# Performance work log

Hardware: AMD Instinct MI355X
Metric: run time of the kernel (lower is better)

Reference implementation:

```python
import jax, jax.numpy as jnp
import numpy as np

B, T, U, V1 = 8, 256, 64, 1024  # V1 = vocab_size + 1 (blank at index 0)
BLANK = 0


def setup_inputs() -> dict:
    key = jax.random.key(0)
    k1, k2, k3, k4 = jax.random.split(key, 4)
    logits = jax.random.normal(k1, (B, T, U + 1, V1), jnp.float32)
    logit_lens = jax.random.randint(k2, (B,), T // 2, T + 1, jnp.int32)
    # target labels must never be the blank index (0)
    y = jax.random.randint(k3, (B, U), 1, V1, jnp.int32)
    y_lens = jax.random.randint(k4, (B,), U // 2, U + 1, jnp.int32)
    return {"logits": logits, "logit_lens": logit_lens, "y": y, "y_lens": y_lens}


def _rnnt_loss(logits, logit_lens, y, y_lens):
    """RNN-Transducer loss (forward-variable DP), reduction='mean' as in warprnnt."""
    b_, t_, u1, _ = logits.shape
    u_ = u1 - 1
    lp = jax.nn.log_softmax(logits, axis=-1)           # [B,T,U+1,V1]
    lp_blank = lp[..., BLANK]                          # [B,T,U+1]
    idx = jnp.broadcast_to(y[:, None, :, None], (b_, t_, u_, 1)).astype(jnp.int32)
    lp_label = jnp.take_along_axis(lp[:, :, :u_, :], idx, axis=3)[..., 0]  # [B,T,U]

    # alpha[0, u] = sum_{k<u} lp_label[0, k]
    alpha0 = jnp.concatenate(
        [jnp.zeros((b_, 1), lp.dtype), jnp.cumsum(lp_label[:, 0, :], axis=1)], axis=1
    )  # [B, U+1]

    def tstep(alpha_prev, xs):
        blank_prev, lab_t = xs                  # [B,U+1], [B,U]
        fb = alpha_prev + blank_prev            # come-from-blank term

        def ustep(carry, uxs):
            fb_u, lab_u = uxs                   # [B], [B]
            new = jnp.logaddexp(fb_u, carry + lab_u)
            return new, new

        _, rest = jax.lax.scan(ustep, fb[:, 0], (fb[:, 1:].T, lab_t.T))  # [U,B]
        alpha_new = jnp.concatenate([fb[:, :1], rest.T], axis=1)         # [B,U+1]
        return alpha_new, alpha_new

    xs = (jnp.moveaxis(lp_blank[:, :-1, :], 1, 0), jnp.moveaxis(lp_label[:, 1:, :], 1, 0))
    _, alphas = jax.lax.scan(tstep, alpha0, xs)          # [T-1,B,U+1]
    all_alpha = jnp.concatenate([alpha0[None], alphas], axis=0)  # [T,B,U+1]

    b_idx = jnp.arange(b_)
    t_idx = logit_lens.astype(jnp.int32) - 1
    u_idx = y_lens.astype(jnp.int32)
    log_like = all_alpha[t_idx, b_idx, u_idx] + lp_blank[b_idx, t_idx, u_idx]
    return -jnp.mean(log_like)


def reference(logits, logit_lens, y, y_lens):
    return _rnnt_loss(logits.astype(jnp.float32), logit_lens, y, y_lens)
```

## Files before the change

### kernel.cpp

```cpp
#include <hip/hip_runtime.h>
#include <math.h>

#define BB 8
#define TT 256
#define UU 64
#define U1 65
#define VV 1024

#define DD 320
#define BSTRIDE_BLANK (DD*U1)
#define BSTRIDE_LAB   (DD*UU)

#define LOG2E 1.4426950408889634f
#define LN2   0.6931471805599453f

__global__ __launch_bounds__(256) void k_rowsoftmax(
    const float* __restrict__ logits,
    const int* __restrict__ y,
    float* __restrict__ blankD,
    float* __restrict__ labD)
{
    const int lane = threadIdx.x & 63;
    const int r = (blockIdx.x * blockDim.x + threadIdx.x) >> 6;
    const int b   = r / (TT * U1);
    const int rem = r - b * (TT * U1);
    const int t   = rem / U1;
    const int u   = rem - t * U1;

    const float* row = logits + (size_t)r * VV;

    float labv = 0.f;
    if (lane == 0 && u < UU) {
        int yidx = y[b * UU + u];
        labv = row[yidx];
    }

    const float4* row4 = (const float4*)row;
    float4 x0 = row4[lane];
    float4 x1 = row4[lane + 64];
    float4 x2 = row4[lane + 128];
    float4 x3 = row4[lane + 192];

    float m = fmaxf(fmaxf(fmaxf(x0.x, x0.y), fmaxf(x0.z, x0.w)),
                    fmaxf(fmaxf(x1.x, x1.y), fmaxf(x1.z, x1.w)));
    m = fmaxf(m, fmaxf(fmaxf(fmaxf(x2.x, x2.y), fmaxf(x2.z, x2.w)),
                       fmaxf(fmaxf(x3.x, x3.y), fmaxf(x3.z, x3.w))));
    #pragma unroll
    for (int off = 32; off; off >>= 1)
        m = fmaxf(m, __shfl_xor(m, off));

    float s = __expf(x0.x - m) + __expf(x0.y - m) + __expf(x0.z - m) + __expf(x0.w - m)
            + __expf(x1.x - m) + __expf(x1.y - m) + __expf(x1.z - m) + __expf(x1.w - m)
            + __expf(x2.x - m) + __expf(x2.y - m) + __expf(x2.z - m) + __expf(x2.w - m)
            + __expf(x3.x - m) + __expf(x3.y - m) + __expf(x3.z - m) + __expf(x3.w - m);
    #pragma unroll
    for (int off = 32; off; off >>= 1)
        s += __shfl_xor(s, off);

    const float lse = m + __logf(s);

    if (lane == 0) {
        const int d = t + u;
        blankD[b * BSTRIDE_BLANK + d * U1 + u] = (x0.x - lse) * LOG2E;
        if (u < UU)
            labD[b * BSTRIDE_LAB + d * UU + u] = (labv - lse) * LOG2E;
    }
}

#define PF 8

__global__ __launch_bounds__(512) void k_dp(
    const float* __restrict__ blankD,
    const float* __restrict__ labD,
    const int* __restrict__ logit_lens,
    const int* __restrict__ y_lens,
    float* __restrict__ out,
    int out_floats)
{
    const int lane = threadIdx.x & 63;
    const int b    = threadIdx.x >> 6;

    const float* pb = blankD + b * BSTRIDE_BLANK;
    const float* pl = labD   + b * BSTRIDE_LAB;

    const int t_idx = logit_lens[b] - 1;
    const int u_idx = y_lens[b];
    const int u     = lane + 1;
    const int dmax  = t_idx + u_idx;

    float cur = pl[lane * (UU + 1)];
    #pragma unroll
    for (int off = 1; off < 64; off <<= 1) {
        float tv = __shfl_up(cur, off);
        if (lane >= off) cur += tv;
    }

    float a0 = 0.f;
    const float fin_blank = pb[dmax * U1 + u_idx];
    float ll = 0.f;

    float rb[PF], rl[PF], r0[PF];
    #pragma unroll
    for (int i = 0; i < PF; ++i) {
        rb[i] = pb[(1 + i) * U1 + u];
        rl[i] = pl[(1 + i) * UU + lane];
        r0[i] = pb[i * U1];
    }

    const int niter = dmax - 1;
    const int nout  = (niter + PF - 1) / PF;
    int d = 2;
    for (int blk = 0; blk < nout; ++blk) {
        #pragma unroll
        for (int i = 0; i < PF; ++i, ++d) {
            int pr = d + PF - 1;
            if (pr > DD - 1) pr = DD - 1;
            const float nb = pb[pr * U1 + u];
            const float nl = pl[pr * UU + lane];
            const float n0 = pb[(pr - 1) * U1];

            if (d <= dmax) {
                a0 += r0[i];

                float left = __shfl_up(cur, 1);
                if (lane == 0) left = a0;

                const int t = d - u;
                if (t >= 1 && t <= TT - 1) {
                    const float aa = cur  + rb[i];
                    const float bv = left + rl[i];
                    const float mm = fmaxf(aa, bv);
                    const float df = fabsf(aa - bv);
                    cur = mm + __log2f(1.0f + exp2f(-df));
                }

                if (t == t_idx && lane == u_idx - 1)
                    ll = cur + fin_blank;
            }
            rb[i] = nb; rl[i] = nl; r0[i] = n0;
        }
    }

    __shared__ float part[BB];
    if (lane == u_idx - 1) part[b] = ll * LN2;
    __syncthreads();
    if (threadIdx.x == 0) {
        float s = 0.f;
        #pragma unroll
        for (int i = 0; i < BB; ++i) s += part[i];
        out[0] = -s * (1.0f / BB);
    }
    for (int i = 1 + (int)threadIdx.x; i < out_floats; i += 512)
        out[i] = 0.f;
}

extern "C" void kernel_launch(void* const* d_in, const int* in_sizes, int n_in,
                              void* d_out, int out_size, void* d_ws, size_t ws_size,
                              hipStream_t stream) {
    const float* logits     = (const float*)d_in[0];
    const int*   logit_lens = (const int*)d_in[1];
    const int*   y          = (const int*)d_in[2];
    const int*   y_lens     = (const int*)d_in[3];
    float*       out        = (float*)d_out;

    float* blankD = (float*)d_ws;
    float* labD   = blankD + BB * BSTRIDE_BLANK;

    const int rows = BB * TT * U1;
    k_rowsoftmax<<<rows / 4, 256, 0, stream>>>(logits, y, blankD, labD);
    k_dp<<<1, 512, 0, stream>>>(blankD, labD, logit_lens, y_lens, out, out_size);
}
```

Measured before the change: 729.2 us.

## Fuse softmax and DP into one kernel with sentinel-based streaming dependencies

Merges the row log-softmax and the anti-diagonal DP into a single launch. Block 0 runs the DP and spin-waits on sentinel-initialised workspace entries, while the other blocks produce blank and label log-probs in t-major order so early diagonals arrive first. A prefill kernel writes the sentinels, and the prefetch depth grows from 8 to 12. The aim is to overlap the serial DP with the bandwidth-bound softmax. The risks are spin-polling overhead, block 0 possibly not being scheduled first, and dependence on forward progress of the producer blocks.

```diff
diff --git a/kernel.cpp b/kernel.cpp
--- a/kernel.cpp
+++ b/kernel.cpp
@@ -13,73 +13,87 @@
 
 #define LOG2E 1.4426950408889634f
 #define LN2   0.6931471805599453f
-
-__global__ __launch_bounds__(256) void k_rowsoftmax(
+#define SENT  0xFFFFFFFFu
+
+#define PF   12
+#define ROWS (BB*TT*U1)
+#define RPB  8
+#define NSMBLK (ROWS/RPB)
+
+__device__ __forceinline__ float agload(const float* p) {
+    return __hip_atomic_load((float*)p, __ATOMIC_RELAXED, __HIP_MEMORY_SCOPE_AGENT);
+}
+__device__ __forceinline__ void agstore(float* p, float v) {
+    __hip_atomic_store(p, v, __ATOMIC_RELAXED, __HIP_MEMORY_SCOPE_AGENT);
+}
+
+__global__ __launch_bounds__(256) void k_prefill(unsigned int* ws) {
+    const int i = blockIdx.x * 256 + threadIdx.x;
+    const int n = BB * (BSTRIDE_BLANK + BSTRIDE_LAB);
+    if (i < n)
+        __hip_atomic_store(ws + i, SENT, __ATOMIC_RELAXED, __HIP_MEMORY_SCOPE_AGENT);
+}
+
+__global__ __launch_bounds__(512) void k_fused(
     const float* __restrict__ logits,
     const int* __restrict__ y,
     float* __restrict__ blankD,
-    float* __restrict__ labD)
-{
-    const int lane = threadIdx.x & 63;
-    const int r = (blockIdx.x * blockDim.x + threadIdx.x) >> 6;
-    const int b   = r / (TT * U1);
-    const int rem = r - b * (TT * U1);
-    const int t   = rem / U1;
-    const int u   = rem - t * U1;
-
-    const float* row = logits + (size_t)r * VV;
-
-    float labv = 0.f;
-    if (lane == 0 && u < UU) {
-        int yidx = y[b * UU + u];
-        labv = row[yidx];
-    }
-
-    const float4* row4 = (const float4*)row;
-    float4 x0 = row4[lane];
-    float4 x1 = row4[lane + 64];
-    float4 x2 = row4[lane + 128];
-    float4 x3 = row4[lane + 192];
-
-    float m = fmaxf(fmaxf(fmaxf(x0.x, x0.y), fmaxf(x0.z, x0.w)),
-                    fmaxf(fmaxf(x1.x, x1.y), fmaxf(x1.z, x1.w)));
-    m = fmaxf(m, fmaxf(fmaxf(fmaxf(x2.x, x2.y), fmaxf(x2.z, x2.w)),
-                       fmaxf(fmaxf(x3.x, x3.y), fmaxf(x3.z, x3.w))));
-    #pragma unroll
-    for (int off = 32; off; off >>= 1)
-        m = fmaxf(m, __shfl_xor(m, off));
-
-    float s = __expf(x0.x - m) + __expf(x0.y - m) + __expf(x0.z - m) + __expf(x0.w - m)
-            + __expf(x1.x - m) + __expf(x1.y - m) + __expf(x1.z - m) + __expf(x1.w - m)
-            + __expf(x2.x - m) + __expf(x2.y - m) + __expf(x2.z - m) + __expf(x2.w - m)
-            + __expf(x3.x - m) + __expf(x3.y - m) + __expf(x3.z - m) + __expf(x3.w - m);
-    #pragma unroll
-    for (int off = 32; off; off >>= 1)
-        s += __shfl_xor(s, off);
-
-    const float lse = m + __logf(s);
-
-    if (lane == 0) {
-        const int d = t + u;
-        blankD[b * BSTRIDE_BLANK + d * U1 + u] = (x0.x - lse) * LOG2E;
-        if (u < UU)
-            labD[b * BSTRIDE_LAB + d * UU + u] = (labv - lse) * LOG2E;
-    }
-}
-
-#define PF 8
-
-__global__ __launch_bounds__(512) void k_dp(
-    const float* __restrict__ blankD,
-    const float* __restrict__ labD,
+    float* __restrict__ labD,
     const int* __restrict__ logit_lens,
     const int* __restrict__ y_lens,
     float* __restrict__ out,
     int out_floats)
 {
     const int lane = threadIdx.x & 63;
-    const int b    = threadIdx.x >> 6;
-
+    const int wv   = threadIdx.x >> 6;
+
+    if (blockIdx.x != 0) {
+        const int rid = (blockIdx.x - 1) * RPB + wv;
+        const int t   = rid / (U1 * BB);
+        const int rem = rid - t * (U1 * BB);
+        const int u   = rem >> 3;
+        const int b   = rem & 7;
+
+        const float* row = logits + (size_t)((b * TT + t) * U1 + u) * VV;
+
+        float labv = 0.f;
+        if (lane == 0 && u < UU)
+            labv = row[y[b * UU + u]];
+
+        const float4* row4 = (const float4*)row;
+        float4 x0 = row4[lane];
+        float4 x1 = row4[lane + 64];
+        float4 x2 = row4[lane + 128];
+        float4 x3 = row4[lane + 192];
+
+        float m = fmaxf(fmaxf(fmaxf(x0.x, x0.y), fmaxf(x0.z, x0.w)),
+                        fmaxf(fmaxf(x1.x, x1.y), fmaxf(x1.z, x1.w)));
+        m = fmaxf(m, fmaxf(fmaxf(fmaxf(x2.x, x2.y), fmaxf(x2.z, x2.w)),
+                           fmaxf(fmaxf(x3.x, x3.y), fmaxf(x3.z, x3.w))));
+        #pragma unroll
+        for (int off = 32; off; off >>= 1)
+            m = fmaxf(m, __shfl_xor(m, off));
+
+        float s = __expf(x0.x - m) + __expf(x0.y - m) + __expf(x0.z - m) + __expf(x0.w - m)
+                + __expf(x1.x - m) + __expf(x1.y - m) + __expf(x1.z - m) + __expf(x1.w - m)
+                + __expf(x2.x - m) + __expf(x2.y - m) + __expf(x2.z - m) + __expf(x2.w - m)
+                + __expf(x3.x - m) + __expf(x3.y - m) + __expf(x3.z - m) + __expf(x3.w - m);
+        #pragma unroll
+        for (int off = 32; off; off >>= 1)
+            s += __shfl_xor(s, off);
+
+        const float lse = m + __logf(s);
+
+        if (lane == 0) {
+            const int d = t + u;
+            agstore(&blankD[b * BSTRIDE_BLANK + d * U1 + u], (x0.x - lse) * LOG2E);
+            if (u < UU)
+                agstore(&labD[b * BSTRIDE_LAB + d * UU + u], (labv - lse) * LOG2E);
+        }
+        return;
+    }
+
+    const int b = wv;
     const float* pb = blankD + b * BSTRIDE_BLANK;
     const float* pl = labD   + b * BSTRIDE_LAB;
 
@@ -88,23 +102,23 @@
     const int u     = lane + 1;
     const int dmax  = t_idx + u_idx;
 
-    float cur = pl[lane * (UU + 1)];
+    float cur = agload(pl + lane * (UU + 1));
+    while (__any(__float_as_uint(cur) == SENT))
+        cur = agload(pl + lane * (UU + 1));
     #pragma unroll
     for (int off = 1; off < 64; off <<= 1) {
         float tv = __shfl_up(cur, off);
         if (lane >= off) cur += tv;
     }
 
-    float a0 = 0.f;
-    const float fin_blank = pb[dmax * U1 + u_idx];
-    float ll = 0.f;
+    float a0 = 0.f, llv = 0.f;
 
     float rb[PF], rl[PF], r0[PF];
     #pragma unroll
     for (int i = 0; i < PF; ++i) {
-        rb[i] = pb[(1 + i) * U1 + u];
-        rl[i] = pl[(1 + i) * UU + lane];
-        r0[i] = pb[i * U1];
+        rb[i] = agload(pb + (1 + i) * U1 + u);
+        rl[i] = agload(pl + (1 + i) * UU + lane);
+        r0[i] = agload(pb + i * U1);
     }
 
     const int niter = dmax - 1;
@@ -115,18 +129,35 @@
         for (int i = 0; i < PF; ++i, ++d) {
             int pr = d + PF - 1;
             if (pr > DD - 1) pr = DD - 1;
-            const float nb = pb[pr * U1 + u];
-            const float nl = pl[pr * UU + lane];
-            const float n0 = pb[(pr - 1) * U1];
+            const float nb = agload(pb + pr * U1 + u);
+            const float nl = agload(pl + pr * UU + lane);
+            const float n0 = agload(pb + (pr - 1) * U1);
 
             if (d <= dmax) {
-                a0 += r0[i];
+                const int t = d - u;
+                const bool need = (t >= 1) && (t <= TT - 1);
+                const bool need0 = (d <= TT);
+
+                unsigned bad = 0;
+                if (need)  bad |= (__float_as_uint(rb[i]) == SENT) |
+                                  (__float_as_uint(rl[i]) == SENT);
+                if (need0) bad |= (__float_as_uint(r0[i]) == SENT);
+                while (__any(bad)) {
+                    rb[i] = agload(pb + (d - 1) * U1 + u);
+                    rl[i] = agload(pl + (d - 1) * UU + lane);
+                    r0[i] = agload(pb + (d - 2) * U1);
+                    bad = 0;
+                    if (need)  bad |= (__float_as_uint(rb[i]) == SENT) |
+                                      (__float_as_uint(rl[i]) == SENT);
+                    if (need0) bad |= (__float_as_uint(r0[i]) == SENT);
+                }
+
+                if (need0) a0 += r0[i];
 
                 float left = __shfl_up(cur, 1);
                 if (lane == 0) left = a0;
 
-                const int t = d - u;
-                if (t >= 1 && t <= TT - 1) {
+                if (need) {
                     const float aa = cur  + rb[i];
                     const float bv = left + rl[i];
                     const float mm = fmaxf(aa, bv);
@@ -135,14 +166,18 @@
                 }
 
                 if (t == t_idx && lane == u_idx - 1)
-                    ll = cur + fin_blank;
+                    llv = cur;
             }
             rb[i] = nb; rl[i] = nl; r0[i] = n0;
         }
     }
 
+    float fb = agload(pb + dmax * U1 + u_idx);
+    while (__any(__float_as_uint(fb) == SENT))
+        fb = agload(pb + dmax * U1 + u_idx);
+
     __shared__ float part[BB];
-    if (lane == u_idx - 1) part[b] = ll * LN2;
+    if (lane == u_idx - 1) part[b] = (llv + fb) * LN2;
     __syncthreads();
     if (threadIdx.x == 0) {
         float s = 0.f;
@@ -166,7 +201,8 @@
     float* blankD = (float*)d_ws;
     float* labD   = blankD + BB * BSTRIDE_BLANK;
 
-    const int rows = BB * TT * U1;
-    k_rowsoftmax<<<rows / 4, 256, 0, stream>>>(logits, y, blankD, labD);
-    k_dp<<<1, 512, 0, stream>>>(blankD, labD, logit_lens, y_lens, out, out_size);
-}
+    const int nsent = BB * (BSTRIDE_BLANK + BSTRIDE_LAB);
+    k_prefill<<<(nsent + 255) / 256, 256, 0, stream>>>((unsigned int*)d_ws);
+    k_fused<<<NSMBLK + 1, 512, 0, stream>>>(logits, y, blankD, labD,
+                                            logit_lens, y_lens, out, out_size);
+}
```

Measured after the change: 712.7 us. -2.3%, faster.
